# Performance work log

Hardware: AMD Instinct MI355X
Metric: run time of the kernel (lower is better)

Reference implementation:

```python
import jax, jax.numpy as jnp
import numpy as np

MODEL_SIZE = 1024
NUM_LAYERS = 8
HEADS = 16
MAX_LENGTH = 4096


def make_alibi_mask(heads, max_len):
    # grid[q,k] = k - q
    grid = (np.arange(max_len)[None, :] - np.arange(max_len)[:, None]).astype(np.float32)
    grid = np.broadcast_to(grid[None, :, :], (heads, max_len, max_len)).copy()
    head_mults = np.power(2.0, -np.linspace(0.0, 8.0, num=heads + 1)[1:]).astype(np.float32)
    grid *= head_mults[:, None, None]
    causal = np.tril(np.ones((max_len, max_len), dtype=np.float32))[None]
    grid = np.where(causal == 0, np.float32(-90000000.0), grid)
    return jnp.asarray(grid)


def layer_norm(x, gamma, beta, eps=1e-3):
    # keras LayerNormalization default epsilon=1e-3
    mu = jnp.mean(x, axis=-1, keepdims=True)
    var = jnp.var(x, axis=-1, keepdims=True)
    return (x - mu) * jax.lax.rsqrt(var + eps) * gamma + beta


def setup_inputs() -> dict:
    key = jax.random.key(0)
    ks = jax.random.split(key, 1 + NUM_LAYERS)
    B, S, D = 2, 2048, MODEL_SIZE
    x = jax.random.normal(ks[0], (B, S, D), dtype=jnp.float32)

    def dense(k, din, dout):
        k1, k2 = jax.random.split(k)
        lim = (6.0 / (din + dout)) ** 0.5
        W = jax.random.uniform(k1, (din, dout), jnp.float32, -lim, lim)
        b = jnp.zeros((dout,), jnp.float32)
        return W, b

    params = []
    for i in range(NUM_LAYERS):
        lk = jax.random.split(ks[1 + i], 5)
        wq, bq = dense(lk[0], D, D)
        wkv, bkv = dense(lk[1], D, 2 * D)
        wo, bo = dense(lk[2], D, D)
        w1, b1 = dense(lk[3], D, 4 * D)
        w2, b2 = dense(lk[4], 4 * D, D)
        ln_att = (jnp.ones((D,), jnp.float32), jnp.zeros((D,), jnp.float32))
        ln_ffn = (jnp.ones((D,), jnp.float32), jnp.zeros((D,), jnp.float32))
        params.append((wq, bq, wkv, bkv, wo, bo, w1, b1, w2, b2,
                       ln_att[0], ln_att[1], ln_ffn[0], ln_ffn[1]))
    final_ln = (jnp.ones((D,), jnp.float32), jnp.zeros((D,), jnp.float32))
    # flatten params into dict
    out = {"target_sequence": x, "final_gamma": final_ln[0], "final_beta": final_ln[1]}
    names = ["wq", "bq", "wkv", "bkv", "wo", "bo", "w1", "b1", "w2", "b2",
             "att_gamma", "att_beta", "ffn_gamma", "ffn_beta"]
    for j, n in enumerate(names):
        out[n] = jnp.stack([params[i][j] for i in range(NUM_LAYERS)])
    return out


def attention(x, wq, bq, wkv, bkv, wo, bo, mask):
    B, S, D = x.shape
    H = HEADS
    hd = D // H
    q = (x @ wq + bq).reshape(B, S, H, hd)
    kv = x @ wkv + bkv
    k, v = jnp.split(kv, 2, axis=-1)
    k = k.reshape(B, S, H, hd)
    v = v.reshape(B, S, H, hd)
    score = jnp.einsum("bqhd,bkhd->bhqk", q, k) * (1.0 / np.sqrt(hd))
    score = score + mask[None]
    attn = jax.nn.softmax(score, axis=-1)
    heads = jnp.einsum("bhqk,bkhd->bqhd", attn, v).reshape(B, S, D)
    return heads @ wo + bo


def reference(target_sequence, wq, bq, wkv, bkv, wo, bo, w1, b1, w2, b2,
              att_gamma, att_beta, ffn_gamma, ffn_beta, final_gamma, final_beta):
    S = target_sequence.shape[1]
    mask = make_alibi_mask(HEADS, MAX_LENGTH)[:, :S, :S]
    x = target_sequence
    for i in range(NUM_LAYERS):
        h = layer_norm(x, att_gamma[i], att_beta[i])
        x = x + attention(h, wq[i], bq[i], wkv[i], bkv[i], wo[i], bo[i], mask)
        h = layer_norm(x, ffn_gamma[i], ffn_beta[i])
        h = jax.nn.softplus(h @ w1[i] + b1[i]) @ w2[i] + b2[i]
        x = x + h
    return layer_norm(x, final_gamma, final_beta)
```

## Files before the change

### kernel.cpp

```cpp
#include <hip/hip_runtime.h>
#include <math.h>

#define DM 1024
#define SEQ 2048
#define BATCH 2
#define NHEAD 16
#define HDIM 64
#define NLAYER 8
#define FFDIM 4096
#define MROWS (BATCH*SEQ)
#define QSTR 3072

typedef __attribute__((ext_vector_type(8))) unsigned short short8;
typedef __attribute__((ext_vector_type(8))) __bf16 bf16x8;
typedef __attribute__((ext_vector_type(4))) float f32x4;

__device__ __forceinline__ float softplus_f(float x){
    const float t = __expf(-fabsf(x));
    return fmaxf(x, 0.0f) + __logf(1.0f + t);
}

__device__ __forceinline__ unsigned short f2bf(float f){
    unsigned u = __builtin_bit_cast(unsigned, f);
    u += 0x7fffu + ((u >> 16) & 1u);
    return (unsigned short)(u >> 16);
}

__device__ __forceinline__ void gload_lds16(const void* g, void* l){
    __builtin_amdgcn_global_load_lds(
        (const __attribute__((address_space(1))) unsigned int*)g,
        (__attribute__((address_space(3))) unsigned int*)l, 16, 0, 0);
}

__global__ __launch_bounds__(256) void tcast_kernel(
    const float* __restrict__ src, unsigned short* __restrict__ dst, int K, int N)
{
    __shared__ float tile[32][33];
    const int bn = blockIdx.x * 32, bk = blockIdx.y * 32;
    const int tx = threadIdx.x & 31, ty = threadIdx.x >> 5;
    #pragma unroll
    for (int i = 0; i < 32; i += 8)
        tile[ty + i][tx] = src[(size_t)(bk + ty + i) * N + bn + tx];
    __syncthreads();
    #pragma unroll
    for (int i = 0; i < 32; i += 8)
        dst[(size_t)(bn + ty + i) * K + bk + tx] = f2bf(tile[tx][ty + i]);
}

__global__ __launch_bounds__(256) void bias_concat_kernel(
    const float* __restrict__ bq, const float* __restrict__ bkv, float* __restrict__ dst)
{
    const int i = blockIdx.x * 256 + threadIdx.x;
    const int l = i / QSTR, c = i % QSTR;
    dst[i] = (c < DM) ? bq[l * DM + c] : bkv[l * 2 * DM + (c - DM)];
}

__global__ __launch_bounds__(256) void vtrans_kernel(
    const unsigned short* __restrict__ qkv, unsigned short* __restrict__ vt)
{
    __shared__ unsigned short tile[64][72];
    const int b  = blockIdx.z;
    const int c0 = blockIdx.x * 64;
    const int s0 = blockIdx.y * 64;
    const int r  = threadIdx.x >> 2;
    const int cq = (threadIdx.x & 3) * 16;
    {
        const unsigned short* src = qkv + (size_t)(b*SEQ + s0 + r) * QSTR + 2*DM + c0 + cq;
        *(uint4*)&tile[r][cq]     = *(const uint4*)(src);
        *(uint4*)&tile[r][cq + 8] = *(const uint4*)(src + 8);
    }
    __syncthreads();
    unsigned short tmp[16];
    #pragma unroll
    for (int j = 0; j < 16; j++) tmp[j] = tile[cq + j][r];
    unsigned short* dst = vt + (size_t)(b*DM + c0 + r) * SEQ + s0 + cq;
    *(uint4*)(dst)     = *(const uint4*)&tmp[0];
    *(uint4*)(dst + 8) = *(const uint4*)&tmp[8];
}

template<bool OUT_BF16>
__global__ __launch_bounds__(256) void ln_kernel(
    const float* __restrict__ x, const float* __restrict__ gamma,
    const float* __restrict__ beta, void* __restrict__ outv)
{
    const int row = blockIdx.x;
    const int t = threadIdx.x;
    const float4 v = ((const float4*)(x + (size_t)row * DM))[t];
    float s  = v.x + v.y + v.z + v.w;
    float s2 = v.x*v.x + v.y*v.y + v.z*v.z + v.w*v.w;
    #pragma unroll
    for (int off = 32; off > 0; off >>= 1){
        s  += __shfl_down(s,  off);
        s2 += __shfl_down(s2, off);
    }
    __shared__ float red[8];
    const int wid = t >> 6;
    if ((t & 63) == 0){ red[wid] = s; red[4 + wid] = s2; }
    __syncthreads();
    if (t == 0){
        red[0] = red[0] + red[1] + red[2] + red[3];
        red[4] = red[4] + red[5] + red[6] + red[7];
    }
    __syncthreads();
    const float mean = red[0] * (1.0f / DM);
    const float var  = red[4] * (1.0f / DM) - mean * mean;
    const float rstd = rsqrtf(var + 1e-3f);
    const float4 g  = ((const float4*)gamma)[t];
    const float4 bt = ((const float4*)beta)[t];
    float ox = (v.x - mean) * rstd * g.x + bt.x;
    float oy = (v.y - mean) * rstd * g.y + bt.y;
    float oz = (v.z - mean) * rstd * g.z + bt.z;
    float ow = (v.w - mean) * rstd * g.w + bt.w;
    if (OUT_BF16){
        ushort4 o = make_ushort4(f2bf(ox), f2bf(oy), f2bf(oz), f2bf(ow));
        *(ushort4*)((unsigned short*)outv + (size_t)row * DM + t*4) = o;
    } else {
        ((float4*)((float*)outv + (size_t)row * DM))[t] = make_float4(ox, oy, oz, ow);
    }
}

template<bool SOFTPLUS, bool RESIDUAL, bool OUT_BF16>
__global__ __launch_bounds__(256, 2) void gemm_bf16_kernel(
    const unsigned short* __restrict__ A, const unsigned short* __restrict__ Bt,
    const float* __restrict__ bias, const float* __restrict__ resid,
    void* __restrict__ Cv, int N, int K)
{
    __shared__ __align__(16) unsigned short As[2][128 * 64];
    __shared__ __align__(16) unsigned short Bs[2][128 * 64];
    const int t = threadIdx.x;
    const int lane = t & 63, w = t >> 6;

    const int gx = gridDim.x;
    const int nwg = gx * gridDim.y;
    int bid = blockIdx.x + gx * blockIdx.y;
    bid = (bid & 7) * (nwg >> 3) + (bid >> 3);
    const int bm = (bid / gx) * 128, bn = (bid % gx) * 128;

    const int srow  = w*8 + (lane >> 3);
    const int sslot = (lane & 7) ^ (lane >> 3);
    const unsigned short* a_g = A  + (size_t)(bm + srow) * K + sslot * 8;
    const unsigned short* b_g = Bt + (size_t)(bn + srow) * K + sslot * 8;

    const int wr = (w >> 1) * 64;
    const int wc = (w & 1) * 64;
    const int fm = lane & 15;
    const int q  = lane >> 4;
    const int f7 = fm & 7;

    f32x4 acc[4][4] = {};
    const int ntile = K >> 6;

#define STAGE(buf, k0)                                                      \
    do {                                                                    \
        _Pragma("unroll")                                                   \
        for (int j = 0; j < 4; j++){                                        \
            gload_lds16(a_g + (size_t)(j*32)*K + (k0), &As[buf][(j*32 + w*8)*64]); \
            gload_lds16(b_g + (size_t)(j*32)*K + (k0), &Bs[buf][(j*32 + w*8)*64]); \
        }                                                                   \
    } while (0)

#define LOADFRAGS(buf)                                                      \
    _Pragma("unroll")                                                       \
    for (int kk2 = 0; kk2 < 2; kk2++){                                      \
        _Pragma("unroll")                                                   \
        for (int mi = 0; mi < 4; mi++)                                      \
            af[kk2][mi] = __builtin_bit_cast(bf16x8, *(const short8*)       \
                &As[buf][(wr + mi*16 + fm)*64 + (((kk2*4 + q) ^ f7) << 3)]);\
        _Pragma("unroll")                                                   \
        for (int ni = 0; ni < 4; ni++)                                      \
            bfm[kk2][ni] = __builtin_bit_cast(bf16x8, *(const short8*)      \
                &Bs[buf][(wc + ni*16 + fm)*64 + (((kk2*4 + q) ^ f7) << 3)]);\
    }

#define MFMAS()                                                             \
    _Pragma("unroll")                                                       \
    for (int kk2 = 0; kk2 < 2; kk2++)                                       \
        _Pragma("unroll")                                                   \
        for (int mi = 0; mi < 4; mi++)                                      \
            _Pragma("unroll")                                               \
            for (int ni = 0; ni < 4; ni++)                                  \
                acc[mi][ni] = __builtin_amdgcn_mfma_f32_16x16x32_bf16(      \
                    af[kk2][mi], bfm[kk2][ni], acc[mi][ni], 0, 0, 0);

    STAGE(0, 0);
    STAGE(1, 64);

    int cur = 0;
    for (int td = 0; td < ntile - 1; ++td){
        asm volatile("s_waitcnt vmcnt(8)" ::: "memory");
        __builtin_amdgcn_s_barrier();
        bf16x8 af[2][4], bfm[2][4];
        LOADFRAGS(cur);
        asm volatile("s_waitcnt lgkmcnt(0)" ::: "memory");
        __builtin_amdgcn_s_barrier();
        if (td + 2 < ntile) STAGE(cur, (td + 2) * 64);
        MFMAS();
        cur ^= 1;
    }
    {
        asm volatile("s_waitcnt vmcnt(0)" ::: "memory");
        __builtin_amdgcn_s_barrier();
        bf16x8 af[2][4], bfm[2][4];
        LOADFRAGS(cur);
        MFMAS();
    }
#undef STAGE
#undef LOADFRAGS
#undef MFMAS

    const int crow = (lane >> 4) * 4;
    const int ccol = lane & 15;
    #pragma unroll
    for (int mi = 0; mi < 4; mi++){
        #pragma unroll
        for (int r = 0; r < 4; r++){
            const size_t row = (size_t)bm + wr + mi*16 + crow + r;
            #pragma unroll
            for (int ni = 0; ni < 4; ni++){
                const int col = bn + wc + ni*16 + ccol;
                float v = acc[mi][ni][r] + bias[col];
                if (SOFTPLUS) v = softplus_f(v);
                if (RESIDUAL) v += resid[row * N + col];
                if (OUT_BF16) ((unsigned short*)Cv)[row * N + col] = f2bf(v);
                else          ((float*)Cv)[row * N + col] = v;
            }
        }
    }
}

__global__ __launch_bounds__(256, 4) void attn_kernel(
    const unsigned short* __restrict__ qkv,
    const unsigned short* __restrict__ vt,
    unsigned short* __restrict__ outg)
{
    __shared__ __align__(16) unsigned short Qs[64][72];
    __shared__ __align__(16) unsigned short Ks[64][72];
    __shared__ __align__(16) unsigned short Vt[64][72];
    __shared__ __align__(16) unsigned short Ps[64][72];

    const int L   = blockIdx.x + 32 * (blockIdx.y + 16 * blockIdx.z);
    const int rep = L >> 8, jj = L & 255;
    const int mm  = jj >> 4, h = jj & 15;
    const int b   = rep >> 1;
    const int qt  = (rep & 1) ? (31 - mm) : mm;

    const int t = threadIdx.x;
    const int lane = t & 63, w = t >> 6;
    const int g = lane >> 4, s = lane & 15;

    const size_t qrow0 = (size_t)(b * SEQ + qt * 64);
    const int srow = t >> 2, slc = t & 3;

    {
        const unsigned short* src = qkv + (qrow0 + srow) * QSTR + h*HDIM + slc*16;
        *(uint4*)&Qs[srow][slc*16]     = *(const uint4*)(src);
        *(uint4*)&Qs[srow][slc*16 + 8] = *(const uint4*)(src + 8);
    }
    __syncthreads();
    bf16x8 qf0 = __builtin_bit_cast(bf16x8, *(const short8*)&Qs[w*16 + s][g*8]);
    bf16x8 qf1 = __builtin_bit_cast(bf16x8, *(const short8*)&Qs[w*16 + s][32 + g*8]);

    const float LOG2E  = 1.4426950408889634f;
    const float qscale = 0.125f * LOG2E;
    const float slope  = exp2f(-0.5f * (float)(h + 1)) * LOG2E;
    const int qi = qt*64 + w*16 + s;
    float m_i = -1e30f, l_i = 0.0f;
    f32x4 accO[4] = {};

    const unsigned short* vbase = vt + (size_t)(b*DM + h*HDIM + srow) * SEQ;

    for (int kt = 0; kt <= qt; kt++){
        __syncthreads();
        {
            const unsigned short* src =
                qkv + (size_t)(b*SEQ + kt*64 + srow) * QSTR + DM + h*HDIM + slc*16;
            *(uint4*)&Ks[srow][slc*16]     = *(const uint4*)(src);
            *(uint4*)&Ks[srow][slc*16 + 8] = *(const uint4*)(src + 8);
        }
        {
            const unsigned short* src = vbase + kt*64 + slc*16;
            *(uint4*)&Vt[srow][slc*16]     = *(const uint4*)(src);
            *(uint4*)&Vt[srow][slc*16 + 8] = *(const uint4*)(src + 8);
        }
        __syncthreads();

        f32x4 sacc[4] = {};
        #pragma unroll
        for (int mi = 0; mi < 4; mi++){
            bf16x8 kf0 = __builtin_bit_cast(bf16x8, *(const short8*)&Ks[mi*16 + s][g*8]);
            bf16x8 kf1 = __builtin_bit_cast(bf16x8, *(const short8*)&Ks[mi*16 + s][32 + g*8]);
            sacc[mi] = __builtin_amdgcn_mfma_f32_16x16x32_bf16(kf0, qf0, sacc[mi], 0, 0, 0);
            sacc[mi] = __builtin_amdgcn_mfma_f32_16x16x32_bf16(kf1, qf1, sacc[mi], 0, 0, 0);
        }

        float sc[16];
        const float bb = slope * (float)(kt*64 - qi);
        #pragma unroll
        for (int mi = 0; mi < 4; mi++)
            #pragma unroll
            for (int r = 0; r < 4; r++)
                sc[mi*4 + r] = fmaf(sacc[mi][r], qscale,
                                    fmaf(slope, (float)(mi*16 + g*4 + r), bb));
        if (kt == qt){
            #pragma unroll
            for (int mi = 0; mi < 4; mi++)
                #pragma unroll
                for (int r = 0; r < 4; r++)
                    if (mi*16 + g*4 + r > w*16 + s) sc[mi*4 + r] = -1e30f;
        }
        float mloc = sc[0];
        #pragma unroll
        for (int e = 1; e < 16; e++) mloc = fmaxf(mloc, sc[e]);
        mloc = fmaxf(mloc, __shfl_xor(mloc, 16));
        mloc = fmaxf(mloc, __shfl_xor(mloc, 32));

        float nm;
        if (__all(mloc - m_i <= 8.0f)){
            nm = m_i;
        } else {
            nm = fmaxf(m_i, mloc);
            const float alpha = exp2f(m_i - nm);
            m_i = nm;
            float av[4];
            #pragma unroll
            for (int r = 0; r < 4; r++) av[r] = __shfl(alpha, g*4 + r);
            #pragma unroll
            for (int ni = 0; ni < 4; ni++)
                #pragma unroll
                for (int r = 0; r < 4; r++) accO[ni][r] *= av[r];
            l_i *= alpha;
        }

        float rsum = 0.0f;
        #pragma unroll
        for (int mi = 0; mi < 4; mi++){
            const float p0 = exp2f(sc[mi*4+0] - nm);
            const float p1 = exp2f(sc[mi*4+1] - nm);
            const float p2 = exp2f(sc[mi*4+2] - nm);
            const float p3 = exp2f(sc[mi*4+3] - nm);
            rsum += (p0 + p1) + (p2 + p3);
            *(ushort4*)&Ps[w*16 + s][mi*16 + g*4] =
                make_ushort4(f2bf(p0), f2bf(p1), f2bf(p2), f2bf(p3));
        }
        rsum += __shfl_xor(rsum, 16);
        rsum += __shfl_xor(rsum, 32);
        l_i += rsum;

        bf16x8 pf0 = __builtin_bit_cast(bf16x8, *(const short8*)&Ps[w*16 + s][g*8]);
        bf16x8 pf1 = __builtin_bit_cast(bf16x8, *(const short8*)&Ps[w*16 + s][32 + g*8]);
        #pragma unroll
        for (int ni = 0; ni < 4; ni++){
            bf16x8 vf0 = __builtin_bit_cast(bf16x8, *(const short8*)&Vt[ni*16 + s][g*8]);
            bf16x8 vf1 = __builtin_bit_cast(bf16x8, *(const short8*)&Vt[ni*16 + s][32 + g*8]);
            accO[ni] = __builtin_amdgcn_mfma_f32_16x16x32_bf16(pf0, vf0, accO[ni], 0, 0, 0);
            accO[ni] = __builtin_amdgcn_mfma_f32_16x16x32_bf16(pf1, vf1, accO[ni], 0, 0, 0);
        }
    }

    float lv[4];
    #pragma unroll
    for (int r = 0; r < 4; r++) lv[r] = 1.0f / __shfl(l_i, g*4 + r);
    #pragma unroll
    for (int ni = 0; ni < 4; ni++)
        #pragma unroll
        for (int r = 0; r < 4; r++)
            outg[(qrow0 + w*16 + g*4 + r) * DM + h*HDIM + ni*16 + s] =
                f2bf(accO[ni][r] * lv[r]);
}

extern "C" void kernel_launch(void* const* d_in, const int* in_sizes, int n_in,
                              void* d_out, int out_size, void* d_ws, size_t ws_size,
                              hipStream_t stream)
{
    (void)in_sizes; (void)n_in; (void)out_size; (void)ws_size;

    const float* x_in = (const float*)d_in[0];
    const float* fg   = (const float*)d_in[1];
    const float* fb   = (const float*)d_in[2];
    const float* wq   = (const float*)d_in[3];
    const float* bq   = (const float*)d_in[4];
    const float* wkv  = (const float*)d_in[5];
    const float* bkv  = (const float*)d_in[6];
    const float* wo   = (const float*)d_in[7];
    const float* bo   = (const float*)d_in[8];
    const float* w1   = (const float*)d_in[9];
    const float* b1   = (const float*)d_in[10];
    const float* w2   = (const float*)d_in[11];
    const float* b2   = (const float*)d_in[12];
    const float* attg = (const float*)d_in[13];
    const float* attb = (const float*)d_in[14];
    const float* ffng = (const float*)d_in[15];
    const float* ffnb = (const float*)d_in[16];

    float* x = (float*)d_out;

    char* wp = (char*)d_ws;
    unsigned short* qkvbuf = (unsigned short*)wp; wp += (size_t)MROWS*QSTR*2;
    unsigned short* h1buf  = (unsigned short*)wp; wp += (size_t)MROWS*FFDIM*2;
    unsigned short* hbuf   = (unsigned short*)wp; wp += (size_t)MROWS*DM*2;
    unsigned short* attbuf = (unsigned short*)wp; wp += (size_t)MROWS*DM*2;
    unsigned short* wt_qkv = (unsigned short*)wp; wp += (size_t)QSTR*DM*2;
    unsigned short* wt_o   = (unsigned short*)wp; wp += (size_t)DM*DM*2;
    unsigned short* wt_1   = (unsigned short*)wp; wp += (size_t)FFDIM*DM*2;
    unsigned short* wt_2   = (unsigned short*)wp; wp += (size_t)DM*FFDIM*2;
    float*          qkv_b  = (float*)wp;          wp += (size_t)NLAYER*QSTR*4;

    unsigned short* vtbuf = h1buf;

    hipMemcpyAsync(x, x_in, (size_t)MROWS*DM*sizeof(float),
                   hipMemcpyDeviceToDevice, stream);
    bias_concat_kernel<<<NLAYER*QSTR/256, 256, 0, stream>>>(bq, bkv, qkv_b);

    const dim3 blk(256);
    const dim3 g_qkv(QSTR/128,  MROWS/128);
    const dim3 g_sq (DM/128,    MROWS/128);
    const dim3 g_ff (FFDIM/128, MROWS/128);
    const dim3 g_at (SEQ/64, NHEAD, BATCH);
    const dim3 g_vt (DM/64, SEQ/64, BATCH);

    for (int i = 0; i < NLAYER; i++){
        const float* wq_i  = wq  + (size_t)i*DM*DM;
        const float* wkv_i = wkv + (size_t)i*DM*2*DM;
        const float* wo_i  = wo  + (size_t)i*DM*DM;
        const float* bo_i  = bo  + (size_t)i*DM;
        const float* w1_i  = w1  + (size_t)i*DM*FFDIM;
        const float* b1_i  = b1  + (size_t)i*FFDIM;
        const float* w2_i  = w2  + (size_t)i*FFDIM*DM;
        const float* b2_i  = b2  + (size_t)i*DM;

        tcast_kernel<<<dim3(DM/32,    DM/32),    blk, 0, stream>>>(wq_i,  wt_qkv,         DM,    DM);
        tcast_kernel<<<dim3(2*DM/32,  DM/32),    blk, 0, stream>>>(wkv_i, wt_qkv + DM*DM, DM,    2*DM);
        tcast_kernel<<<dim3(DM/32,    DM/32),    blk, 0, stream>>>(wo_i,  wt_o,           DM,    DM);
        tcast_kernel<<<dim3(FFDIM/32, DM/32),    blk, 0, stream>>>(w1_i,  wt_1,           DM,    FFDIM);
        tcast_kernel<<<dim3(DM/32,    FFDIM/32), blk, 0, stream>>>(w2_i,  wt_2,           FFDIM, DM);

        ln_kernel<true><<<MROWS, blk, 0, stream>>>(x, attg + (size_t)i*DM, attb + (size_t)i*DM, hbuf);
        gemm_bf16_kernel<false,false,true><<<g_qkv, blk, 0, stream>>>(
            hbuf, wt_qkv, qkv_b + (size_t)i*QSTR, nullptr, qkvbuf, QSTR, DM);
        vtrans_kernel<<<g_vt, blk, 0, stream>>>(qkvbuf, vtbuf);
        attn_kernel<<<g_at, blk, 0, stream>>>(qkvbuf, vtbuf, attbuf);
        gemm_bf16_kernel<false,true,false><<<g_sq, blk, 0, stream>>>(
            attbuf, wt_o, bo_i, x, x, DM, DM);
        ln_kernel<true><<<MROWS, blk, 0, stream>>>(x, ffng + (size_t)i*DM, ffnb + (size_t)i*DM, hbuf);
        gemm_bf16_kernel<true,false,true><<<g_ff, blk, 0, stream>>>(
            hbuf, wt_1, b1_i, nullptr, h1buf, FFDIM, DM);
        gemm_bf16_kernel<false,true,false><<<g_sq, blk, 0, stream>>>(
            h1buf, wt_2, b2_i, x, x, DM, FFDIM);
    }
    ln_kernel<false><<<MROWS, blk, 0, stream>>>(x, fg, fb, x);
}
```

Measured before the change: 2.268 ms.

## Batch all-layer weight transpose-cast, prefetch K/V in attention, pack bf16 conversion

When the workspace is large enough, all eight layers' weights are transposed and cast to bf16 in a single launch before the layer loop. This replaces forty small per-layer kernel launches and keeps the GEMMs from waiting on them, at the cost of a larger workspace. The attention kernel now prefetches the next K/V tile into registers while computing on the current one. It also uses a tree max reduction and a packed v_cvt_pk_bf16_f32 instruction to convert probabilities. The prefetch adds register pressure, and the packed conversion may round differently from the manual f2bf.

```diff
diff --git a/kernel.cpp b/kernel.cpp
--- a/kernel.cpp
+++ b/kernel.cpp
@@ -10,6 +10,7 @@
 #define FFDIM 4096
 #define MROWS (BATCH*SEQ)
 #define QSTR 3072
+#define LWT (12*DM*DM)
 
 typedef __attribute__((ext_vector_type(8))) unsigned short short8;
 typedef __attribute__((ext_vector_type(8))) __bf16 bf16x8;
@@ -37,6 +38,38 @@
 {
     __shared__ float tile[32][33];
     const int bn = blockIdx.x * 32, bk = blockIdx.y * 32;
+    const int tx = threadIdx.x & 31, ty = threadIdx.x >> 5;
+    #pragma unroll
+    for (int i = 0; i < 32; i += 8)
+        tile[ty + i][tx] = src[(size_t)(bk + ty + i) * N + bn + tx];
+    __syncthreads();
+    #pragma unroll
+    for (int i = 0; i < 32; i += 8)
+        dst[(size_t)(bn + ty + i) * K + bk + tx] = f2bf(tile[tx][ty + i]);
+}
+
+__global__ __launch_bounds__(256) void tcast_all_kernel(
+    const float* __restrict__ wq, const float* __restrict__ wkv,
+    const float* __restrict__ wo, const float* __restrict__ w1,
+    const float* __restrict__ w2, unsigned short* __restrict__ wt)
+{
+    const int l = blockIdx.y;
+    int tb = blockIdx.x;
+    const float* src; unsigned short* dst; int K, N;
+    if (tb < 1024){
+        src = wq + (size_t)l*DM*DM;            dst = wt + (size_t)l*LWT;            K = DM;    N = DM;
+    } else if (tb < 3072){ tb -= 1024;
+        src = wkv + (size_t)l*2*DM*DM;         dst = wt + (size_t)l*LWT + DM*DM;    K = DM;    N = 2*DM;
+    } else if (tb < 4096){ tb -= 3072;
+        src = wo + (size_t)l*DM*DM;            dst = wt + (size_t)l*LWT + 3*DM*DM;  K = DM;    N = DM;
+    } else if (tb < 8192){ tb -= 4096;
+        src = w1 + (size_t)l*DM*FFDIM;         dst = wt + (size_t)l*LWT + 4*DM*DM;  K = DM;    N = FFDIM;
+    } else {               tb -= 8192;
+        src = w2 + (size_t)l*DM*FFDIM;         dst = wt + (size_t)l*LWT + 8*DM*DM;  K = FFDIM; N = DM;
+    }
+    const int nx = N >> 5;
+    const int bn = (tb % nx) * 32, bk = (tb / nx) * 32;
+    __shared__ float tile[32][33];
     const int tx = threadIdx.x & 31, ty = threadIdx.x >> 5;
     #pragma unroll
     for (int i = 0; i < 32; i += 8)
@@ -251,6 +284,17 @@
     const size_t qrow0 = (size_t)(b * SEQ + qt * 64);
     const int srow = t >> 2, slc = t & 3;
 
+    const unsigned short* vbase = vt + (size_t)(b*DM + h*HDIM + srow) * SEQ;
+
+    uint4 kreg0, kreg1, vreg0, vreg1;
+    {
+        const unsigned short* ks =
+            qkv + (size_t)(b*SEQ + srow) * QSTR + DM + h*HDIM + slc*16;
+        kreg0 = *(const uint4*)ks; kreg1 = *(const uint4*)(ks + 8);
+        const unsigned short* vs = vbase + slc*16;
+        vreg0 = *(const uint4*)vs; vreg1 = *(const uint4*)(vs + 8);
+    }
+
     {
         const unsigned short* src = qkv + (qrow0 + srow) * QSTR + h*HDIM + slc*16;
         *(uint4*)&Qs[srow][slc*16]     = *(const uint4*)(src);
@@ -267,22 +311,21 @@
     float m_i = -1e30f, l_i = 0.0f;
     f32x4 accO[4] = {};
 
-    const unsigned short* vbase = vt + (size_t)(b*DM + h*HDIM + srow) * SEQ;
-
     for (int kt = 0; kt <= qt; kt++){
         __syncthreads();
-        {
-            const unsigned short* src =
-                qkv + (size_t)(b*SEQ + kt*64 + srow) * QSTR + DM + h*HDIM + slc*16;
-            *(uint4*)&Ks[srow][slc*16]     = *(const uint4*)(src);
-            *(uint4*)&Ks[srow][slc*16 + 8] = *(const uint4*)(src + 8);
-        }
-        {
-            const unsigned short* src = vbase + kt*64 + slc*16;
-            *(uint4*)&Vt[srow][slc*16]     = *(const uint4*)(src);
-            *(uint4*)&Vt[srow][slc*16 + 8] = *(const uint4*)(src + 8);
-        }
+        *(uint4*)&Ks[srow][slc*16]     = kreg0;
+        *(uint4*)&Ks[srow][slc*16 + 8] = kreg1;
+        *(uint4*)&Vt[srow][slc*16]     = vreg0;
+        *(uint4*)&Vt[srow][slc*16 + 8] = vreg1;
         __syncthreads();
+
+        if (kt < qt){
+            const unsigned short* ks =
+                qkv + (size_t)(b*SEQ + (kt+1)*64 + srow) * QSTR + DM + h*HDIM + slc*16;
+            kreg0 = *(const uint4*)ks; kreg1 = *(const uint4*)(ks + 8);
+            const unsigned short* vs = vbase + (kt+1)*64 + slc*16;
+            vreg0 = *(const uint4*)vs; vreg1 = *(const uint4*)(vs + 8);
+        }
 
         f32x4 sacc[4] = {};
         #pragma unroll
@@ -308,9 +351,12 @@
                 for (int r = 0; r < 4; r++)
                     if (mi*16 + g*4 + r > w*16 + s) sc[mi*4 + r] = -1e30f;
         }
-        float mloc = sc[0];
-        #pragma unroll
-        for (int e = 1; e < 16; e++) mloc = fmaxf(mloc, sc[e]);
+        float m8[8];
+        #pragma unroll
+        for (int e = 0; e < 8; e++) m8[e] = fmaxf(sc[e], sc[e + 8]);
+        float m4a = fmaxf(m8[0], m8[4]), m4b = fmaxf(m8[1], m8[5]);
+        float m4c = fmaxf(m8[2], m8[6]), m4d = fmaxf(m8[3], m8[7]);
+        float mloc = fmaxf(fmaxf(m4a, m4b), fmaxf(m4c, m4d));
         mloc = fmaxf(mloc, __shfl_xor(mloc, 16));
         mloc = fmaxf(mloc, __shfl_xor(mloc, 32));
 
@@ -339,8 +385,10 @@
             const float p2 = exp2f(sc[mi*4+2] - nm);
             const float p3 = exp2f(sc[mi*4+3] - nm);
             rsum += (p0 + p1) + (p2 + p3);
-            *(ushort4*)&Ps[w*16 + s][mi*16 + g*4] =
-                make_ushort4(f2bf(p0), f2bf(p1), f2bf(p2), f2bf(p3));
+            unsigned r0, r1;
+            asm("v_cvt_pk_bf16_f32 %0, %1, %2" : "=v"(r0) : "v"(p0), "v"(p1));
+            asm("v_cvt_pk_bf16_f32 %0, %1, %2" : "=v"(r1) : "v"(p2), "v"(p3));
+            *(uint2*)&Ps[w*16 + s][mi*16 + g*4] = make_uint2(r0, r1);
         }
         rsum += __shfl_xor(rsum, 16);
         rsum += __shfl_xor(rsum, 32);
@@ -372,7 +420,7 @@
                               void* d_out, int out_size, void* d_ws, size_t ws_size,
                               hipStream_t stream)
 {
-    (void)in_sizes; (void)n_in; (void)out_size; (void)ws_size;
+    (void)in_sizes; (void)n_in; (void)out_size;
 
     const float* x_in = (const float*)d_in[0];
     const float* fg   = (const float*)d_in[1];
@@ -399,17 +447,28 @@
     unsigned short* h1buf  = (unsigned short*)wp; wp += (size_t)MROWS*FFDIM*2;
     unsigned short* hbuf   = (unsigned short*)wp; wp += (size_t)MROWS*DM*2;
     unsigned short* attbuf = (unsigned short*)wp; wp += (size_t)MROWS*DM*2;
-    unsigned short* wt_qkv = (unsigned short*)wp; wp += (size_t)QSTR*DM*2;
-    unsigned short* wt_o   = (unsigned short*)wp; wp += (size_t)DM*DM*2;
-    unsigned short* wt_1   = (unsigned short*)wp; wp += (size_t)FFDIM*DM*2;
-    unsigned short* wt_2   = (unsigned short*)wp; wp += (size_t)DM*FFDIM*2;
     float*          qkv_b  = (float*)wp;          wp += (size_t)NLAYER*QSTR*4;
+
+    const bool big = ws_size >= ((size_t)280 << 20);
+    unsigned short* wt_all = nullptr;
+    unsigned short *wt_qkv = nullptr, *wt_o = nullptr, *wt_1 = nullptr, *wt_2 = nullptr;
+    if (big){
+        wt_all = (unsigned short*)wp; wp += (size_t)NLAYER*LWT*2;
+    } else {
+        wt_qkv = (unsigned short*)wp; wp += (size_t)QSTR*DM*2;
+        wt_o   = (unsigned short*)wp; wp += (size_t)DM*DM*2;
+        wt_1   = (unsigned short*)wp; wp += (size_t)FFDIM*DM*2;
+        wt_2   = (unsigned short*)wp; wp += (size_t)DM*FFDIM*2;
+    }
 
     unsigned short* vtbuf = h1buf;
 
     hipMemcpyAsync(x, x_in, (size_t)MROWS*DM*sizeof(float),
                    hipMemcpyDeviceToDevice, stream);
     bias_concat_kernel<<<NLAYER*QSTR/256, 256, 0, stream>>>(bq, bkv, qkv_b);
+    if (big)
+        tcast_all_kernel<<<dim3(12288, NLAYER), 256, 0, stream>>>(
+            wq, wkv, wo, w1, w2, wt_all);
 
     const dim3 blk(256);
     const dim3 g_qkv(QSTR/128,  MROWS/128);
@@ -419,33 +478,35 @@
     const dim3 g_vt (DM/64, SEQ/64, BATCH);
 
     for (int i = 0; i < NLAYER; i++){
-        const float* wq_i  = wq  + (size_t)i*DM*DM;
-        const float* wkv_i = wkv + (size_t)i*DM*2*DM;
-        const float* wo_i  = wo  + (size_t)i*DM*DM;
         const float* bo_i  = bo  + (size_t)i*DM;
-        const float* w1_i  = w1  + (size_t)i*DM*FFDIM;
         const float* b1_i  = b1  + (size_t)i*FFDIM;
-        const float* w2_i  = w2  + (size_t)i*FFDIM*DM;
         const float* b2_i  = b2  + (size_t)i*DM;
 
-        tcast_kernel<<<dim3(DM/32,    DM/32),    blk, 0, stream>>>(wq_i,  wt_qkv,         DM,    DM);
-        tcast_kernel<<<dim3(2*DM/32,  DM/32),    blk, 0, stream>>>(wkv_i, wt_qkv + DM*DM, DM,    2*DM);
-        tcast_kernel<<<dim3(DM/32,    DM/32),    blk, 0, stream>>>(wo_i,  wt_o,           DM,    DM);
-        tcast_kernel<<<dim3(FFDIM/32, DM/32),    blk, 0, stream>>>(w1_i,  wt_1,           DM,    FFDIM);
-        tcast_kernel<<<dim3(DM/32,    FFDIM/32), blk, 0, stream>>>(w2_i,  wt_2,           FFDIM, DM);
+        const unsigned short *tq, *to, *t1, *t2;
+        if (big){
+            unsigned short* base = wt_all + (size_t)i*LWT;
+            tq = base; to = base + 3*DM*DM; t1 = base + 4*DM*DM; t2 = base + 8*DM*DM;
+        } else {
+            tcast_kernel<<<dim3(DM/32,    DM/32),    blk, 0, stream>>>(wq  + (size_t)i*DM*DM,    wt_qkv,         DM,    DM);
+            tcast_kernel<<<dim3(2*DM/32,  DM/32),    blk, 0, stream>>>(wkv + (size_t)i*2*DM*DM,  wt_qkv + DM*DM, DM,    2*DM);
+            tcast_kernel<<<dim3(DM/32,    DM/32),    blk, 0, stream>>>(wo  + (size_t)i*DM*DM,    wt_o,           DM,    DM);
+            tcast_kernel<<<dim3(FFDIM/32, DM/32),    blk, 0, stream>>>(w1  + (size_t)i*DM*FFDIM, wt_1,           DM,    FFDIM);
+            tcast_kernel<<<dim3(DM/32,    FFDIM/32), blk, 0, stream>>>(w2  + (size_t)i*DM*FFDIM, wt_2,           FFDIM, DM);
+            tq = wt_qkv; to = wt_o; t1 = wt_1; t2 = wt_2;
+        }
 
         ln_kernel<true><<<MROWS, blk, 0, stream>>>(x, attg + (size_t)i*DM, attb + (size_t)i*DM, hbuf);
         gemm_bf16_kernel<false,false,true><<<g_qkv, blk, 0, stream>>>(
-            hbuf, wt_qkv, qkv_b + (size_t)i*QSTR, nullptr, qkvbuf, QSTR, DM);
+            hbuf, tq, qkv_b + (size_t)i*QSTR, nullptr, qkvbuf, QSTR, DM);
         vtrans_kernel<<<g_vt, blk, 0, stream>>>(qkvbuf, vtbuf);
         attn_kernel<<<g_at, blk, 0, stream>>>(qkvbuf, vtbuf, attbuf);
         gemm_bf16_kernel<false,true,false><<<g_sq, blk, 0, stream>>>(
-            attbuf, wt_o, bo_i, x, x, DM, DM);
+            attbuf, to, bo_i, x, x, DM, DM);
         ln_kernel<true><<<MROWS, blk, 0, stream>>>(x, ffng + (size_t)i*DM, ffnb + (size_t)i*DM, hbuf);
         gemm_bf16_kernel<true,false,true><<<g_ff, blk, 0, stream>>>(
-            hbuf, wt_1, b1_i, nullptr, h1buf, FFDIM, DM);
+            hbuf, t1, b1_i, nullptr, h1buf, FFDIM, DM);
         gemm_bf16_kernel<false,true,false><<<g_sq, blk, 0, stream>>>(
-            h1buf, wt_2, b2_i, x, x, DM, FFDIM);
+            h1buf, t2, b2_i, x, x, DM, FFDIM);
     }
     ln_kernel<false><<<MROWS, blk, 0, stream>>>(x, fg, fb, x);
 }
```

Result: slower. 2.501 ms (+10.3%).
